# Optimization experiments

Hardware: AMD Instinct MI355X
Metric: run time of the kernel (lower is better)

The kernel has to match this reference:

```python
import jax, jax.numpy as jnp
import numpy as np

D_MODEL = 512
NUM_HEADS = 8
D_HEAD = D_MODEL // NUM_HEADS
SCALE = 1.0 / np.sqrt(D_HEAD)


def setup_inputs() -> dict:
    key = jax.random.key(0)
    ks = jax.random.split(key, 16)
    B, T, D = 8, 1024, D_MODEL
    std = 1.0 / np.sqrt(D)
    inp = {
        'x': jax.random.normal(ks[0], (B, T, D), jnp.float32),
        'pos_enc': jax.random.normal(ks[1], (1, 2 * T - 1, D), jnp.float32),
        'Wq': jax.random.normal(ks[2], (D, D), jnp.float32) * std,
        'bq': jnp.zeros((D,), jnp.float32),
        'Wk': jax.random.normal(ks[3], (D, D), jnp.float32) * std,
        'bk': jnp.zeros((D,), jnp.float32),
        'Wv': jax.random.normal(ks[4], (D, D), jnp.float32) * std,
        'bv': jnp.zeros((D,), jnp.float32),
        'Wpos': jax.random.normal(ks[5], (D, D), jnp.float32) * std,
        'pos_bias_u': jax.random.normal(ks[6], (NUM_HEADS, D_HEAD), jnp.float32) * std,
        'pos_bias_v': jax.random.normal(ks[7], (NUM_HEADS, D_HEAD), jnp.float32) * std,
        'Wo': jax.random.normal(ks[8], (D, D), jnp.float32) * std,
        'bo': jnp.zeros((D,), jnp.float32),
    }
    return inp


def _relative_shift(x):
    # x: (batch, heads, time, 2*time-1) -> (batch, heads, time, time)
    b, h, t, _ = x.shape
    x = jnp.pad(x, ((0, 0), (0, 0), (0, 0), (1, 0)))  # (b,h,t,2t)
    x = x.reshape(b, h, 2 * t, t)
    x = x[:, :, 1:, :]
    x = x.reshape(b, h, t, 2 * t - 1)
    return x[:, :, :, :t]


def reference(x, pos_enc, Wq, bq, Wk, bk, Wv, bv, Wpos, pos_bias_u, pos_bias_v, Wo, bo):
    B, T, D = x.shape
    H, Dh = NUM_HEADS, D_HEAD
    q = (x @ Wq + bq).reshape(B, T, H, Dh).transpose(0, 2, 1, 3)  # (B,H,T,Dh)
    k = (x @ Wk + bk).reshape(B, T, H, Dh).transpose(0, 2, 1, 3)
    v = (x @ Wv + bv).reshape(B, T, H, Dh).transpose(0, 2, 1, 3)
    p = (pos_enc @ Wpos).reshape(1, -1, H, Dh).transpose(0, 2, 1, 3)  # (1,H,2T-1,Dh)

    q_u = q + pos_bias_u[None, :, None, :]
    q_v = q + pos_bias_v[None, :, None, :]

    content_score = jnp.einsum('bhtd,bhsd->bhts', q_u, k)         # (B,H,T,T)
    pos_score = jnp.einsum('bhtd,xhpd->bhtp', q_v, p)             # (B,H,T,2T-1)
    pos_score = _relative_shift(pos_score)                         # (B,H,T,T)

    scores = (content_score + pos_score) * SCALE
    attn = jax.nn.softmax(scores, axis=-1)
    out = jnp.einsum('bhts,bhsd->bhtd', attn, v)                   # (B,H,T,Dh)
    out = out.transpose(0, 2, 1, 3).reshape(B, T, D)
    return out @ Wo + bo
```

## Files before the change

kernel.cpp:

```cpp
#include <hip/hip_runtime.h>
#include <hip/hip_bf16.h>

#define T_SEQ 1024
#define D_MODEL 512
#define N_HEADS 8
#define D_HEAD 64
#define KSCALE 0.1803368801111244f

typedef unsigned short ushort_t;
typedef short s16x8 __attribute__((ext_vector_type(8)));
typedef float f32x4 __attribute__((ext_vector_type(4)));

__device__ inline f32x4 mfma16(s16x8 a, s16x8 b, f32x4 c) {
    return __builtin_amdgcn_mfma_f32_16x16x32_bf16(a, b, c, 0, 0, 0);
}

__device__ inline ushort_t f2bf(float f) {
    union { float f; unsigned u; } v; v.f = f;
    unsigned r = v.u + 0x7FFFu + ((v.u >> 16) & 1u);
    return (ushort_t)(r >> 16);
}
__device__ inline float bf2f(short s) {
    union { unsigned u; float f; } t; t.u = ((unsigned)(unsigned short)s) << 16; return t.f;
}
__device__ inline void cvt4(const float4 f, ushort_t* t) {
    t[0] = f2bf(f.x); t[1] = f2bf(f.y); t[2] = f2bf(f.z); t[3] = f2bf(f.w);
}
__device__ inline s16x8 pack8(const ushort_t* t) {
    s16x8 r;
    #pragma unroll
    for (int e = 0; e < 8; ++e) r[e] = (short)t[e];
    return r;
}

__device__ inline int lidx(int row, int chunk) {
    return row * 64 + ((chunk ^ (row & 7)) << 3);
}

__device__ inline void gl_lds16(const ushort_t* g, ushort_t* l) {
    __builtin_amdgcn_global_load_lds(
        (const __attribute__((address_space(1))) unsigned*)g,
        (__attribute__((address_space(3))) unsigned*)l, 16, 0, 0);
}

__global__ __launch_bounds__(256) void prep(
    const float* __restrict__ x, const float* __restrict__ pos,
    const float* __restrict__ W0, const float* __restrict__ W1,
    const float* __restrict__ W2, const float* __restrict__ W3,
    const float* __restrict__ W4,
    ushort_t* __restrict__ xb, ushort_t* __restrict__ posb,
    ushort_t* __restrict__ WT)
{
    __shared__ float T[64][68];
    const int bx = blockIdx.x;
    const int tid = threadIdx.x;
    if (bx < 2560) {
        const size_t N1 = (size_t)8192 * 512;
        size_t e = ((size_t)bx * 256 + tid) * 8;
        ushort_t tmp[8];
        if (e < N1) {
            const float4* s = (const float4*)(x + e);
            cvt4(s[0], tmp); cvt4(s[1], tmp + 4);
            *(s16x8*)(xb + e) = pack8(tmp);
        } else {
            size_t e2 = e - N1;
            int row = (int)(e2 >> 9);
            if (row < 2047) {
                const float4* s = (const float4*)(pos + e2);
                cvt4(s[0], tmp); cvt4(s[1], tmp + 4);
            } else {
                #pragma unroll
                for (int i = 0; i < 8; ++i) tmp[i] = 0;
            }
            *(s16x8*)(posb + e2) = pack8(tmp);
        }
    } else {
        const int bz = bx - 2560;
        const int z = bz >> 6;
        const int rem = bz & 63;
        const int n0 = (rem & 7) * 64, k0 = (rem >> 3) * 64;
        const float* W = (z == 0) ? W0 : (z == 1) ? W1
                       : (z == 2) ? W2 : (z == 3) ? W3 : W4;
        const int rr = tid >> 2, cc = (tid & 3) * 16;

        const float* src = W + (size_t)(k0 + rr) * 512 + n0 + cc;
        *(float4*)&T[rr][cc + 0]  = *(const float4*)(src);
        *(float4*)&T[rr][cc + 4]  = *(const float4*)(src + 4);
        *(float4*)&T[rr][cc + 8]  = *(const float4*)(src + 8);
        *(float4*)&T[rr][cc + 12] = *(const float4*)(src + 12);
        __syncthreads();

        ushort_t tmp[16];
        #pragma unroll
        for (int e = 0; e < 16; ++e) tmp[e] = f2bf(T[cc + e][rr]);
        ushort_t* dst = WT + ((size_t)z * 512 + n0 + rr) * 512 + k0 + cc;
        *(s16x8*)dst       = pack8(tmp);
        *(s16x8*)(dst + 8) = pack8(tmp + 8);
    }
}

__global__ __launch_bounds__(256) void gemm_qkvp(
    const ushort_t* __restrict__ xb, const ushort_t* __restrict__ posb,
    const ushort_t* __restrict__ WT,
    const float* __restrict__ bq, const float* __restrict__ bk,
    const float* __restrict__ bv, const float* __restrict__ pbu,
    ushort_t* __restrict__ Qu, ushort_t* __restrict__ Ko,
    ushort_t* __restrict__ VoT, ushort_t* __restrict__ Po)
{
    const int tid = threadIdx.x;
    const bool is_p = (blockIdx.x == 12);
    int row0, col0;
    const ushort_t* A;
    const ushort_t* B;
    if (is_p) {
        row0 = ((int)blockIdx.y >> 2) * 128;
        col0 = ((int)blockIdx.y & 3) * 128;
        A = posb;
        B = WT + (size_t)3 * 512 * 512;
    } else {
        row0 = blockIdx.y * 128;
        col0 = blockIdx.x * 128;
        A = xb;
        B = WT;
    }
    const int w = tid >> 6, lane = tid & 63;
    const int quad = lane >> 4, lanelo = lane & 15;
    const int wr = w >> 1, wc = w & 1;

    __shared__ ushort_t AsF[128 * 64];
    __shared__ ushort_t BsF[128 * 64];

    f32x4 acc[4][4] = {};

    for (int k0 = 0; k0 < 512; k0 += 64) {
        __syncthreads();
        #pragma unroll
        for (int i = 0; i < 4; ++i) {
            const int L = i * 256 + tid;
            const int r = L >> 3, j = (L & 7) * 8;
            ushort_t* lbase = AsF + (size_t)(i * 256 + (tid & ~63)) * 8;
            gl_lds16(A + (size_t)(row0 + r) * 512 + k0 + j, lbase);
            ushort_t* lbase2 = BsF + (size_t)(i * 256 + (tid & ~63)) * 8;
            gl_lds16(B + (size_t)(col0 + r) * 512 + k0 + j, lbase2);
        }
        __syncthreads();

        #pragma unroll
        for (int ks = 0; ks < 2; ++ks) {
            s16x8 af[4], bf[4];
            #pragma unroll
            for (int i = 0; i < 4; ++i)
                af[i] = *(const s16x8*)(AsF + (size_t)(64 * wr + 16 * i + lanelo) * 64 + ks * 32 + quad * 8);
            #pragma unroll
            for (int j = 0; j < 4; ++j)
                bf[j] = *(const s16x8*)(BsF + (size_t)(64 * wc + 16 * j + lanelo) * 64 + ks * 32 + quad * 8);
            #pragma unroll
            for (int i = 0; i < 4; ++i)
                #pragma unroll
                for (int j = 0; j < 4; ++j)
                    acc[i][j] = mfma16(af[i], bf[j], acc[i][j]);
        }
    }

    if (is_p) {
        #pragma unroll
        for (int j = 0; j < 4; ++j) {
            int c = col0 + 64 * wc + 16 * j + lanelo;
            #pragma unroll
            for (int i = 0; i < 4; ++i)
                #pragma unroll
                for (int r = 0; r < 4; ++r) {
                    int row = row0 + 64 * wr + 16 * i + 4 * quad + r;
                    Po[(size_t)row * 512 + c] = f2bf(acc[i][j][r]);
                }
        }
        return;
    }

    const int set = col0 >> 9;
    const int cbase = (col0 & 511) + 64 * wc;
    if (set == 0) {
        #pragma unroll
        for (int j = 0; j < 4; ++j) {
            int c = cbase + 16 * j + lanelo;
            float vq = bq[c] + pbu[c];
            #pragma unroll
            for (int i = 0; i < 4; ++i)
                #pragma unroll
                for (int r = 0; r < 4; ++r) {
                    int row = row0 + 64 * wr + 16 * i + 4 * quad + r;
                    Qu[(size_t)row * 512 + c] = f2bf((acc[i][j][r] + vq) * KSCALE);
                }
        }
    } else if (set == 1) {
        #pragma unroll
        for (int j = 0; j < 4; ++j) {
            int c = cbase + 16 * j + lanelo;
            float vbk = bk[c];
            #pragma unroll
            for (int i = 0; i < 4; ++i)
                #pragma unroll
                for (int r = 0; r < 4; ++r) {
                    int row = row0 + 64 * wr + 16 * i + 4 * quad + r;
                    Ko[(size_t)row * 512 + c] = f2bf(acc[i][j][r] + vbk);
                }
        }
    } else {
        const int b_idx = row0 >> 10;
        #pragma unroll
        for (int j = 0; j < 4; ++j) {
            int c = cbase + 16 * j + lanelo;
            int hh = c >> 6, d = c & 63;
            float vbb = bv[c];
            #pragma unroll
            for (int i = 0; i < 4; ++i) {
                int t = (row0 & 1023) + 64 * wr + 16 * i + 4 * quad;
                ushort4 vp;
                vp.x = f2bf(acc[i][j][0] + vbb);
                vp.y = f2bf(acc[i][j][1] + vbb);
                vp.z = f2bf(acc[i][j][2] + vbb);
                vp.w = f2bf(acc[i][j][3] + vbb);
                *(ushort4*)(VoT + ((size_t)((b_idx * 8 + hh) * 64 + d)) * 1024 + t) = vp;
            }
        }
    }
}

__global__ __launch_bounds__(256) void attn_mfma(
    const ushort_t* __restrict__ Qu,
    const ushort_t* __restrict__ Kb, const ushort_t* __restrict__ VT,
    const ushort_t* __restrict__ Pb,
    const float* __restrict__ pbu, const float* __restrict__ pbv,
    ushort_t* __restrict__ AOb)
{
    const int tid = threadIdx.x;
    const int t0 = blockIdx.x * 64;
    const int h  = blockIdx.y;
    const int b  = blockIdx.z;
    const int w = tid >> 6, lane = tid & 63;
    const int quad = lane >> 4, lanelo = lane & 15;
    const int sr = tid >> 2;
    const int scch = (tid & 3) * 2;
    const int sc = scch * 8;

    __shared__ ushort_t Kt[64 * 64];
    __shared__ ushort_t VtT[64 * 64];
    __shared__ ushort_t Pt[128 * 64];
    __shared__ ushort_t Ps[64 * 64];

    const size_t qrow = (size_t)(b * T_SEQ + t0 + 16 * w + lanelo) * 512 + h * 64;
    s16x8 qu[2], qv[2];
    qu[0] = *(const s16x8*)(Qu + qrow + quad * 8);
    qu[1] = *(const s16x8*)(Qu + qrow + 32 + quad * 8);
    #pragma unroll
    for (int e = 0; e < 8; ++e) {
        int k0i = h * 64 + quad * 8 + e;
        float d0 = (pbv[k0i] - pbu[k0i]) * KSCALE;
        float d1 = (pbv[k0i + 32] - pbu[k0i + 32]) * KSCALE;
        qv[0][e] = (short)f2bf(bf2f(qu[0][e]) + d0);
        qv[1][e] = (short)f2bf(bf2f(qu[1][e]) + d1);
    }

    f32x4 acc_o[4] = {};
    float l_part[4] = {0.f, 0.f, 0.f, 0.f};

    const int u_base = lanelo + 63 - 4 * quad;
    const ushort_t* VTbh = VT + ((size_t)((b * 8 + h) * 64)) * 1024;
    const ushort_t* Kbh  = Kb + (size_t)b * T_SEQ * 512 + (size_t)h * 64;
    const int pr_base = 960 - t0;

    {
        const ushort_t* kp = Kbh + (size_t)sr * 512 + sc;
        *(s16x8*)(Kt + lidx(sr, scch))     = *(const s16x8*)kp;
        *(s16x8*)(Kt + lidx(sr, scch + 1)) = *(const s16x8*)(kp + 8);
        const ushort_t* vp = VTbh + (size_t)sr * 1024 + sc;
        *(s16x8*)(VtT + lidx(sr, scch))     = *(const s16x8*)vp;
        *(s16x8*)(VtT + lidx(sr, scch + 1)) = *(const s16x8*)(vp + 8);
        const int pr_r = tid >> 1, pc0 = (tid & 1) * 4;
        const int slot = (pr_base + pr_r) & 127;
        const ushort_t* gp = Pb + (size_t)(pr_base + pr_r) * 512 + h * 64 + pc0 * 8;
        *(s16x8*)(Pt + lidx(slot, pc0))     = *(const s16x8*)(gp +  0);
        *(s16x8*)(Pt + lidx(slot, pc0 + 1)) = *(const s16x8*)(gp +  8);
        *(s16x8*)(Pt + lidx(slot, pc0 + 2)) = *(const s16x8*)(gp + 16);
        *(s16x8*)(Pt + lidx(slot, pc0 + 3)) = *(const s16x8*)(gp + 24);
    }

    for (int it = 0; it < 16; ++it) {
        const int s0 = it * 64;
        __syncthreads();

        s16x8 kp0, kp1, vp0, vp1, pp0, pp1;
        const bool more = (it < 15);
        if (more) {
            const ushort_t* kp = Kbh + (size_t)(s0 + 64 + sr) * 512 + sc;
            kp0 = *(const s16x8*)kp;
            kp1 = *(const s16x8*)(kp + 8);
            const ushort_t* vp = VTbh + (size_t)sr * 1024 + s0 + 64 + sc;
            vp0 = *(const s16x8*)vp;
            vp1 = *(const s16x8*)(vp + 8);
            const ushort_t* gp = Pb + (size_t)(pr_base + s0 + 128 + sr) * 512 + h * 64 + sc;
            pp0 = *(const s16x8*)gp;
            pp1 = *(const s16x8*)(gp + 8);
        }

        const int pbase = (pr_base + s0) & 127;
        f32x4 acc_c[4] = {};
        f32x4 acc_g[5] = {};
        #pragma unroll
        for (int ks = 0; ks < 2; ++ks) {
            #pragma unroll
            for (int tn = 0; tn < 4; ++tn) {
                s16x8 kf = *(const s16x8*)(Kt + lidx(tn * 16 + lanelo, 4 * ks + quad));
                acc_c[tn] = mfma16(qu[ks], kf, acc_c[tn]);
            }
            #pragma unroll
            for (int i = 0; i < 5; ++i) {
                int prow = (pbase + (3 - w + i) * 16 + lanelo) & 127;
                s16x8 pf = *(const s16x8*)(Pt + lidx(prow, 4 * ks + quad));
                acc_g[i] = mfma16(qv[ks], pf, acc_g[i]);
            }
        }

        float p[4][4];
        #pragma unroll
        for (int r = 0; r < 4; ++r) {
            int u = u_base - r;
            int srcl = (quad << 4) | (u & 15);
            bool hi = (u >= 64);
            #pragma unroll
            for (int tn = 0; tn < 4; ++tn) {
                float v0 = __shfl(acc_g[tn][r], srcl);
                float v1 = __shfl(acc_g[tn + 1][r], srcl);
                float e = __builtin_amdgcn_exp2f(acc_c[tn][r] + (hi ? v1 : v0));
                p[tn][r] = e;
                l_part[r] += e;
            }
        }
        #pragma unroll
        for (int tn = 0; tn < 4; ++tn)
            #pragma unroll
            for (int r = 0; r < 4; ++r) {
                int pr = 16 * w + 4 * quad + r;
                int ch = 2 * tn + (lanelo >> 3);
                Ps[pr * 64 + ((ch ^ (pr & 7)) << 3) + (lanelo & 7)] = f2bf(p[tn][r]);
            }
        asm volatile("s_waitcnt lgkmcnt(0)" ::: "memory");

        #pragma unroll
        for (int ks = 0; ks < 2; ++ks) {
            s16x8 af = *(const s16x8*)(Ps + lidx(16 * w + lanelo, 4 * ks + quad));
            #pragma unroll
            for (int dt = 0; dt < 4; ++dt) {
                s16x8 vb = *(const s16x8*)(VtT + lidx(dt * 16 + lanelo, 4 * ks + quad));
                acc_o[dt] = mfma16(af, vb, acc_o[dt]);
            }
        }

        __syncthreads();
        if (more) {
            *(s16x8*)(Kt + lidx(sr, scch))      = kp0;
            *(s16x8*)(Kt + lidx(sr, scch + 1))  = kp1;
            *(s16x8*)(VtT + lidx(sr, scch))     = vp0;
            *(s16x8*)(VtT + lidx(sr, scch + 1)) = vp1;
            const int slot = (pr_base + s0 + 128 + sr) & 127;
            *(s16x8*)(Pt + lidx(slot, scch))     = pp0;
            *(s16x8*)(Pt + lidx(slot, scch + 1)) = pp1;
        }
    }

    float inv[4];
    #pragma unroll
    for (int r = 0; r < 4; ++r) {
        float l = l_part[r];
        l += __shfl_xor(l, 1);
        l += __shfl_xor(l, 2);
        l += __shfl_xor(l, 4);
        l += __shfl_xor(l, 8);
        inv[r] = 1.0f / l;
    }

    __syncthreads();
    #pragma unroll
    for (int r = 0; r < 4; ++r)
        #pragma unroll
        for (int dt = 0; dt < 4; ++dt) {
            int pr = 16 * w + 4 * quad + r;
            int ch = 2 * dt + (lanelo >> 3);
            Ps[pr * 64 + ((ch ^ (pr & 7)) << 3) + (lanelo & 7)] = f2bf(acc_o[dt][r] * inv[r]);
        }
    __syncthreads();
    {
        ushort_t* dst = AOb + (size_t)(b * T_SEQ + t0 + sr) * 512 + h * 64 + sc;
        *(s16x8*)dst       = *(const s16x8*)(Ps + lidx(sr, scch));
        *(s16x8*)(dst + 8) = *(const s16x8*)(Ps + lidx(sr, scch + 1));
    }
}

__global__ __launch_bounds__(256) void gemm_out(
    const ushort_t* __restrict__ A, const ushort_t* __restrict__ WTo,
    const float* __restrict__ bias, float* __restrict__ C)
{
    const int tid = threadIdx.x;
    const int col0 = blockIdx.x * 128;
    const int row0 = blockIdx.y * 128;
    const int w = tid >> 6, lane = tid & 63;
    const int quad = lane >> 4, lanelo = lane & 15;
    const int wr = w >> 1, wc = w & 1;

    __shared__ ushort_t AsF[128 * 64];
    __shared__ ushort_t BsF[128 * 64];

    f32x4 acc[4][4] = {};

    for (int k0 = 0; k0 < 512; k0 += 64) {
        __syncthreads();
        #pragma unroll
        for (int i = 0; i < 4; ++i) {
            const int L = i * 256 + tid;
            const int r = L >> 3, j = (L & 7) * 8;
            ushort_t* lbase = AsF + (size_t)(i * 256 + (tid & ~63)) * 8;
            gl_lds16(A + (size_t)(row0 + r) * 512 + k0 + j, lbase);
            ushort_t* lbase2 = BsF + (size_t)(i * 256 + (tid & ~63)) * 8;
            gl_lds16(WTo + (size_t)(col0 + r) * 512 + k0 + j, lbase2);
        }
        __syncthreads();

        #pragma unroll
        for (int ks = 0; ks < 2; ++ks) {
            s16x8 af[4], bf[4];
            #pragma unroll
            for (int i = 0; i < 4; ++i)
                af[i] = *(const s16x8*)(AsF + (size_t)(64 * wr + 16 * i + lanelo) * 64 + ks * 32 + quad * 8);
            #pragma unroll
            for (int j = 0; j < 4; ++j)
                bf[j] = *(const s16x8*)(BsF + (size_t)(64 * wc + 16 * j + lanelo) * 64 + ks * 32 + quad * 8);
            #pragma unroll
            for (int i = 0; i < 4; ++i)
                #pragma unroll
                for (int j = 0; j < 4; ++j)
                    acc[i][j] = mfma16(af[i], bf[j], acc[i][j]);
        }
    }

    #pragma unroll
    for (int j = 0; j < 4; ++j) {
        int c = col0 + 64 * wc + 16 * j + lanelo;
        float vb = bias[c];
        #pragma unroll
        for (int i = 0; i < 4; ++i)
            #pragma unroll
            for (int r = 0; r < 4; ++r) {
                int row = row0 + 64 * wr + 16 * i + 4 * quad + r;
                C[(size_t)row * 512 + c] = acc[i][j][r] + vb;
            }
    }
}

extern "C" void kernel_launch(void* const* d_in, const int* in_sizes, int n_in,
                              void* d_out, int out_size, void* d_ws, size_t ws_size,
                              hipStream_t stream) {
    const float* x       = (const float*)d_in[0];
    const float* pos_enc = (const float*)d_in[1];
    const float* Wq      = (const float*)d_in[2];
    const float* bq      = (const float*)d_in[3];
    const float* Wk      = (const float*)d_in[4];
    const float* bk      = (const float*)d_in[5];
    const float* Wv      = (const float*)d_in[6];
    const float* bv      = (const float*)d_in[7];
    const float* Wpos    = (const float*)d_in[8];
    const float* pbu     = (const float*)d_in[9];
    const float* pbv     = (const float*)d_in[10];
    const float* Wo      = (const float*)d_in[11];
    const float* bo      = (const float*)d_in[12];
    float* out = (float*)d_out;

    const size_t M  = 8 * T_SEQ;
    const size_t SZ = M * D_MODEL;

    char* ws = (char*)d_ws;
    ushort_t* xb   = (ushort_t*)ws;              ws += SZ * 2;
    ushort_t* posb = (ushort_t*)ws;              ws += (size_t)2048 * 512 * 2;
    ushort_t* Qu_b = (ushort_t*)ws;              ws += SZ * 2;
    ushort_t* K_b  = (ushort_t*)ws;              ws += SZ * 2;
    ushort_t* VT_b = (ushort_t*)ws;              ws += SZ * 2;
    ushort_t* P_b  = (ushort_t*)ws;              ws += (size_t)2048 * 512 * 2;
    ushort_t* WT   = (ushort_t*)ws;              ws += (size_t)5 * 512 * 512 * 2;
    ushort_t* AOb  = (ushort_t*)ws;              ws += SZ * 2;

    dim3 blk(256);

    hipLaunchKernelGGL(prep, dim3(2880), blk, 0, stream,
                       x, pos_enc, Wq, Wk, Wv, Wpos, Wo, xb, posb, WT);

    hipLaunchKernelGGL(gemm_qkvp, dim3(13, 64), blk, 0, stream,
                       xb, posb, WT, bq, bk, bv, pbu,
                       Qu_b, K_b, VT_b, P_b);

    hipLaunchKernelGGL(attn_mfma, dim3(16, 8, 8), blk, 0, stream,
                       Qu_b, K_b, VT_b, P_b, pbu, pbv, AOb);

    hipLaunchKernelGGL(gemm_out, dim3(4, 64), blk, 0, stream,
                       AOb, WT + (size_t)4 * 512 * 512, bo, out);
}
```

Before: 207.4 us.

## Enlarge attention query tile, double-buffer K/V/P via direct-to-LDS loads, remap blocks for XCD locality

The attention kernel now processes 128 query rows per block, two 16-row tiles per wave, so each K, V and positional fragment read from LDS feeds twice as many MFMAs. K/V are double-buffered and the positional window is a 256-row ring, both filled by asynchronous global-to-LDS loads instead of staging through registers, which removes one barrier per iteration. MFMA sections are bracketed with s_setprio, and launch bounds request 2 blocks per CU. All three GEMM/attention grids are flattened and remapped so consecutive blocks on the same XCD share data. The trade-off is more LDS and registers per block and half as many attention blocks.

```diff
diff --git a/kernel.cpp b/kernel.cpp
--- a/kernel.cpp
+++ b/kernel.cpp
@@ -108,18 +108,22 @@
     ushort_t* __restrict__ VoT, ushort_t* __restrict__ Po)
 {
     const int tid = threadIdx.x;
-    const bool is_p = (blockIdx.x == 12);
+    const int flat = blockIdx.x;
+    const int nf = (flat & 7) * 104 + (flat >> 3);
+    const int bxi = nf % 13, byi = nf / 13;
+
+    const bool is_p = (bxi == 12);
     int row0, col0;
     const ushort_t* A;
     const ushort_t* B;
     if (is_p) {
-        row0 = ((int)blockIdx.y >> 2) * 128;
-        col0 = ((int)blockIdx.y & 3) * 128;
+        row0 = (byi >> 2) * 128;
+        col0 = (byi & 3) * 128;
         A = posb;
         B = WT + (size_t)3 * 512 * 512;
     } else {
-        row0 = blockIdx.y * 128;
-        col0 = blockIdx.x * 128;
+        row0 = byi * 128;
+        col0 = bxi * 128;
         A = xb;
         B = WT;
     }
@@ -226,7 +230,7 @@
     }
 }
 
-__global__ __launch_bounds__(256) void attn_mfma(
+__global__ __launch_bounds__(256, 2) void attn_mfma(
     const ushort_t* __restrict__ Qu,
     const ushort_t* __restrict__ Kb, const ushort_t* __restrict__ VT,
     const ushort_t* __restrict__ Pb,
@@ -234,165 +238,192 @@
     ushort_t* __restrict__ AOb)
 {
     const int tid = threadIdx.x;
-    const int t0 = blockIdx.x * 64;
-    const int h  = blockIdx.y;
-    const int b  = blockIdx.z;
+    const int flat = blockIdx.x;
+    const int nf = (flat & 7) * 64 + (flat >> 3);
+    const int t0 = (nf & 7) * 128;
+    const int h  = (nf >> 3) & 7;
+    const int b  = nf >> 6;
+
     const int w = tid >> 6, lane = tid & 63;
     const int quad = lane >> 4, lanelo = lane & 15;
-    const int sr = tid >> 2;
-    const int scch = (tid & 3) * 2;
-    const int sc = scch * 8;
-
-    __shared__ ushort_t Kt[64 * 64];
-    __shared__ ushort_t VtT[64 * 64];
-    __shared__ ushort_t Pt[128 * 64];
-    __shared__ ushort_t Ps[64 * 64];
-
-    const size_t qrow = (size_t)(b * T_SEQ + t0 + 16 * w + lanelo) * 512 + h * 64;
-    s16x8 qu[2], qv[2];
-    qu[0] = *(const s16x8*)(Qu + qrow + quad * 8);
-    qu[1] = *(const s16x8*)(Qu + qrow + 32 + quad * 8);
+
+    __shared__ ushort_t Kt[2 * 64 * 64];
+    __shared__ ushort_t VtT[2 * 64 * 64];
+    __shared__ ushort_t Pt[256 * 64];
+    __shared__ ushort_t Ps[128 * 64];
+
+    const size_t qr0 = (size_t)(b * T_SEQ + t0 + 32 * w + lanelo) * 512 + h * 64;
+    s16x8 qu0[2], qu1[2], qv0[2], qv1[2];
+    qu0[0] = *(const s16x8*)(Qu + qr0 + quad * 8);
+    qu0[1] = *(const s16x8*)(Qu + qr0 + 32 + quad * 8);
+    qu1[0] = *(const s16x8*)(Qu + qr0 + (size_t)16 * 512 + quad * 8);
+    qu1[1] = *(const s16x8*)(Qu + qr0 + (size_t)16 * 512 + 32 + quad * 8);
     #pragma unroll
     for (int e = 0; e < 8; ++e) {
         int k0i = h * 64 + quad * 8 + e;
         float d0 = (pbv[k0i] - pbu[k0i]) * KSCALE;
         float d1 = (pbv[k0i + 32] - pbu[k0i + 32]) * KSCALE;
-        qv[0][e] = (short)f2bf(bf2f(qu[0][e]) + d0);
-        qv[1][e] = (short)f2bf(bf2f(qu[1][e]) + d1);
-    }
-
-    f32x4 acc_o[4] = {};
-    float l_part[4] = {0.f, 0.f, 0.f, 0.f};
-
-    const int u_base = lanelo + 63 - 4 * quad;
+        qv0[0][e] = (short)f2bf(bf2f(qu0[0][e]) + d0);
+        qv0[1][e] = (short)f2bf(bf2f(qu0[1][e]) + d1);
+        qv1[0][e] = (short)f2bf(bf2f(qu1[0][e]) + d0);
+        qv1[1][e] = (short)f2bf(bf2f(qu1[1][e]) + d1);
+    }
+
+    f32x4 acc_o[2][4] = {};
+    float l_part[2][4] = {{0.f,0.f,0.f,0.f},{0.f,0.f,0.f,0.f}};
+
     const ushort_t* VTbh = VT + ((size_t)((b * 8 + h) * 64)) * 1024;
     const ushort_t* Kbh  = Kb + (size_t)b * T_SEQ * 512 + (size_t)h * 64;
     const int pr_base = 960 - t0;
 
     {
-        const ushort_t* kp = Kbh + (size_t)sr * 512 + sc;
-        *(s16x8*)(Kt + lidx(sr, scch))     = *(const s16x8*)kp;
-        *(s16x8*)(Kt + lidx(sr, scch + 1)) = *(const s16x8*)(kp + 8);
-        const ushort_t* vp = VTbh + (size_t)sr * 1024 + sc;
-        *(s16x8*)(VtT + lidx(sr, scch))     = *(const s16x8*)vp;
-        *(s16x8*)(VtT + lidx(sr, scch + 1)) = *(const s16x8*)(vp + 8);
-        const int pr_r = tid >> 1, pc0 = (tid & 1) * 4;
-        const int slot = (pr_base + pr_r) & 127;
-        const ushort_t* gp = Pb + (size_t)(pr_base + pr_r) * 512 + h * 64 + pc0 * 8;
-        *(s16x8*)(Pt + lidx(slot, pc0))     = *(const s16x8*)(gp +  0);
-        *(s16x8*)(Pt + lidx(slot, pc0 + 1)) = *(const s16x8*)(gp +  8);
-        *(s16x8*)(Pt + lidx(slot, pc0 + 2)) = *(const s16x8*)(gp + 16);
-        *(s16x8*)(Pt + lidx(slot, pc0 + 3)) = *(const s16x8*)(gp + 24);
-    }
+        #pragma unroll
+        for (int i = 0; i < 2; ++i) {
+            const int L = i * 256 + tid;
+            const int r = L >> 3;
+            const int ch = (L & 7) ^ (r & 7);
+            gl_lds16(Kbh + (size_t)r * 512 + ch * 8,
+                     Kt + (size_t)(i * 256 + (tid & ~63)) * 8);
+            gl_lds16(VTbh + (size_t)r * 1024 + ch * 8,
+                     VtT + (size_t)(i * 256 + (tid & ~63)) * 8);
+        }
+        const int g0p = pr_base - 64;
+        #pragma unroll
+        for (int i = 0; i < 6; ++i) {
+            const int L = i * 256 + tid;
+            const int gr = g0p + (L >> 3);
+            const int ch = (L & 7) ^ (gr & 7);
+            const int sgb = (g0p + ((i * 256 + (tid & ~63)) >> 3)) & 255;
+            gl_lds16(Pb + (size_t)gr * 512 + h * 64 + ch * 8,
+                     Pt + (size_t)sgb * 64);
+        }
+    }
+    __syncthreads();
 
     for (int it = 0; it < 16; ++it) {
         const int s0 = it * 64;
+        const int cur = it & 1;
+
+        if (it < 15) {
+            ushort_t* Kn = Kt + (cur ^ 1) * 4096;
+            ushort_t* Vn = VtT + (cur ^ 1) * 4096;
+            const int sn = s0 + 64;
+            #pragma unroll
+            for (int i = 0; i < 2; ++i) {
+                const int L = i * 256 + tid;
+                const int r = L >> 3;
+                const int ch = (L & 7) ^ (r & 7);
+                gl_lds16(Kbh + (size_t)(sn + r) * 512 + ch * 8,
+                         Kn + (size_t)(i * 256 + (tid & ~63)) * 8);
+                gl_lds16(VTbh + (size_t)r * 1024 + sn + ch * 8,
+                         Vn + (size_t)(i * 256 + (tid & ~63)) * 8);
+            }
+            const int g0 = pr_base + s0 + 128;
+            #pragma unroll
+            for (int i = 0; i < 2; ++i) {
+                const int L = i * 256 + tid;
+                const int gr = g0 + (L >> 3);
+                const int ch = (L & 7) ^ (gr & 7);
+                const int sgb = (g0 + ((i * 256 + (tid & ~63)) >> 3)) & 255;
+                gl_lds16(Pb + (size_t)gr * 512 + h * 64 + ch * 8,
+                         Pt + (size_t)sgb * 64);
+            }
+        }
+
+        const ushort_t* Kc = Kt + cur * 4096;
+        const ushort_t* Vc = VtT + cur * 4096;
+        const int pb = (pr_base + s0) & 255;
+
+        f32x4 acc_c[2][4] = {};
+        f32x4 acc_g[2][5] = {};
+        __builtin_amdgcn_s_setprio(1);
+        #pragma unroll
+        for (int ks = 0; ks < 2; ++ks) {
+            #pragma unroll
+            for (int tn = 0; tn < 4; ++tn) {
+                s16x8 kf = *(const s16x8*)(Kc + lidx(tn * 16 + lanelo, 4 * ks + quad));
+                acc_c[0][tn] = mfma16(qu0[ks], kf, acc_c[0][tn]);
+                acc_c[1][tn] = mfma16(qu1[ks], kf, acc_c[1][tn]);
+            }
+            #pragma unroll
+            for (int m = 0; m < 6; ++m) {
+                int prow = (pb + 256 + (2 - 2 * w + m) * 16 + lanelo) & 255;
+                s16x8 pf = *(const s16x8*)(Pt + lidx(prow, 4 * ks + quad));
+                if (m >= 1) acc_g[0][m - 1] = mfma16(qv0[ks], pf, acc_g[0][m - 1]);
+                if (m <= 4) acc_g[1][m]     = mfma16(qv1[ks], pf, acc_g[1][m]);
+            }
+        }
+        __builtin_amdgcn_s_setprio(0);
+
+        #pragma unroll
+        for (int rt = 0; rt < 2; ++rt) {
+            #pragma unroll
+            for (int r = 0; r < 4; ++r) {
+                const int u = lanelo + 15 - 4 * quad - r;
+                const int srcl = (quad << 4) | (u & 15);
+                const bool hi = (u >= 16);
+                #pragma unroll
+                for (int tn = 0; tn < 4; ++tn) {
+                    float v0 = __shfl(acc_g[rt][tn][r], srcl);
+                    float v1 = __shfl(acc_g[rt][tn + 1][r], srcl);
+                    float e = __builtin_amdgcn_exp2f(acc_c[rt][tn][r] + (hi ? v1 : v0));
+                    l_part[rt][r] += e;
+                    const int pr = 32 * w + 16 * rt + 4 * quad + r;
+                    const int ch = 2 * tn + (lanelo >> 3);
+                    Ps[pr * 64 + ((ch ^ (pr & 7)) << 3) + (lanelo & 7)] = f2bf(e);
+                }
+            }
+        }
+        asm volatile("s_waitcnt lgkmcnt(0)" ::: "memory");
+
+        __builtin_amdgcn_s_setprio(1);
+        #pragma unroll
+        for (int ks = 0; ks < 2; ++ks) {
+            s16x8 af0 = *(const s16x8*)(Ps + lidx(32 * w + lanelo, 4 * ks + quad));
+            s16x8 af1 = *(const s16x8*)(Ps + lidx(32 * w + 16 + lanelo, 4 * ks + quad));
+            #pragma unroll
+            for (int dt = 0; dt < 4; ++dt) {
+                s16x8 vb = *(const s16x8*)(Vc + lidx(dt * 16 + lanelo, 4 * ks + quad));
+                acc_o[0][dt] = mfma16(af0, vb, acc_o[0][dt]);
+                acc_o[1][dt] = mfma16(af1, vb, acc_o[1][dt]);
+            }
+        }
+        __builtin_amdgcn_s_setprio(0);
+
         __syncthreads();
-
-        s16x8 kp0, kp1, vp0, vp1, pp0, pp1;
-        const bool more = (it < 15);
-        if (more) {
-            const ushort_t* kp = Kbh + (size_t)(s0 + 64 + sr) * 512 + sc;
-            kp0 = *(const s16x8*)kp;
-            kp1 = *(const s16x8*)(kp + 8);
-            const ushort_t* vp = VTbh + (size_t)sr * 1024 + s0 + 64 + sc;
-            vp0 = *(const s16x8*)vp;
-            vp1 = *(const s16x8*)(vp + 8);
-            const ushort_t* gp = Pb + (size_t)(pr_base + s0 + 128 + sr) * 512 + h * 64 + sc;
-            pp0 = *(const s16x8*)gp;
-            pp1 = *(const s16x8*)(gp + 8);
-        }
-
-        const int pbase = (pr_base + s0) & 127;
-        f32x4 acc_c[4] = {};
-        f32x4 acc_g[5] = {};
-        #pragma unroll
-        for (int ks = 0; ks < 2; ++ks) {
-            #pragma unroll
-            for (int tn = 0; tn < 4; ++tn) {
-                s16x8 kf = *(const s16x8*)(Kt + lidx(tn * 16 + lanelo, 4 * ks + quad));
-                acc_c[tn] = mfma16(qu[ks], kf, acc_c[tn]);
-            }
-            #pragma unroll
-            for (int i = 0; i < 5; ++i) {
-                int prow = (pbase + (3 - w + i) * 16 + lanelo) & 127;
-                s16x8 pf = *(const s16x8*)(Pt + lidx(prow, 4 * ks + quad));
-                acc_g[i] = mfma16(qv[ks], pf, acc_g[i]);
-            }
-        }
-
-        float p[4][4];
+    }
+
+    float inv[2][4];
+    #pragma unroll
+    for (int rt = 0; rt < 2; ++rt)
         #pragma unroll
         for (int r = 0; r < 4; ++r) {
-            int u = u_base - r;
-            int srcl = (quad << 4) | (u & 15);
-            bool hi = (u >= 64);
-            #pragma unroll
-            for (int tn = 0; tn < 4; ++tn) {
-                float v0 = __shfl(acc_g[tn][r], srcl);
-                float v1 = __shfl(acc_g[tn + 1][r], srcl);
-                float e = __builtin_amdgcn_exp2f(acc_c[tn][r] + (hi ? v1 : v0));
-                p[tn][r] = e;
-                l_part[r] += e;
-            }
-        }
-        #pragma unroll
-        for (int tn = 0; tn < 4; ++tn)
+            float l = l_part[rt][r];
+            l += __shfl_xor(l, 1);
+            l += __shfl_xor(l, 2);
+            l += __shfl_xor(l, 4);
+            l += __shfl_xor(l, 8);
+            inv[rt][r] = 1.0f / l;
+        }
+
+    #pragma unroll
+    for (int rt = 0; rt < 2; ++rt)
+        #pragma unroll
+        for (int dt = 0; dt < 4; ++dt)
             #pragma unroll
             for (int r = 0; r < 4; ++r) {
-                int pr = 16 * w + 4 * quad + r;
-                int ch = 2 * tn + (lanelo >> 3);
-                Ps[pr * 64 + ((ch ^ (pr & 7)) << 3) + (lanelo & 7)] = f2bf(p[tn][r]);
-            }
-        asm volatile("s_waitcnt lgkmcnt(0)" ::: "memory");
-
-        #pragma unroll
-        for (int ks = 0; ks < 2; ++ks) {
-            s16x8 af = *(const s16x8*)(Ps + lidx(16 * w + lanelo, 4 * ks + quad));
-            #pragma unroll
-            for (int dt = 0; dt < 4; ++dt) {
-                s16x8 vb = *(const s16x8*)(VtT + lidx(dt * 16 + lanelo, 4 * ks + quad));
-                acc_o[dt] = mfma16(af, vb, acc_o[dt]);
-            }
-        }
-
-        __syncthreads();
-        if (more) {
-            *(s16x8*)(Kt + lidx(sr, scch))      = kp0;
-            *(s16x8*)(Kt + lidx(sr, scch + 1))  = kp1;
-            *(s16x8*)(VtT + lidx(sr, scch))     = vp0;
-            *(s16x8*)(VtT + lidx(sr, scch + 1)) = vp1;
-            const int slot = (pr_base + s0 + 128 + sr) & 127;
-            *(s16x8*)(Pt + lidx(slot, scch))     = pp0;
-            *(s16x8*)(Pt + lidx(slot, scch + 1)) = pp1;
-        }
-    }
-
-    float inv[4];
-    #pragma unroll
-    for (int r = 0; r < 4; ++r) {
-        float l = l_part[r];
-        l += __shfl_xor(l, 1);
-        l += __shfl_xor(l, 2);
-        l += __shfl_xor(l, 4);
-        l += __shfl_xor(l, 8);
-        inv[r] = 1.0f / l;
-    }
-
-    __syncthreads();
-    #pragma unroll
-    for (int r = 0; r < 4; ++r)
-        #pragma unroll
-        for (int dt = 0; dt < 4; ++dt) {
-            int pr = 16 * w + 4 * quad + r;
-            int ch = 2 * dt + (lanelo >> 3);
-            Ps[pr * 64 + ((ch ^ (pr & 7)) << 3) + (lanelo & 7)] = f2bf(acc_o[dt][r] * inv[r]);
-        }
+                const int pr = 32 * w + 16 * rt + 4 * quad + r;
+                const int ch = 2 * dt + (lanelo >> 3);
+                Ps[pr * 64 + ((ch ^ (pr & 7)) << 3) + (lanelo & 7)] =
+                    f2bf(acc_o[rt][dt][r] * inv[rt][r]);
+            }
     __syncthreads();
     {
-        ushort_t* dst = AOb + (size_t)(b * T_SEQ + t0 + sr) * 512 + h * 64 + sc;
-        *(s16x8*)dst       = *(const s16x8*)(Ps + lidx(sr, scch));
-        *(s16x8*)(dst + 8) = *(const s16x8*)(Ps + lidx(sr, scch + 1));
+        const int row = tid >> 1, cb = (tid & 1) * 4;
+        ushort_t* dst = AOb + (size_t)(b * T_SEQ + t0 + row) * 512 + h * 64 + cb * 8;
+        #pragma unroll
+        for (int c = 0; c < 4; ++c)
+            *(s16x8*)(dst + c * 8) = *(const s16x8*)(Ps + lidx(row, cb + c));
     }
 }
 
@@ -401,8 +432,10 @@
     const float* __restrict__ bias, float* __restrict__ C)
 {
     const int tid = threadIdx.x;
-    const int col0 = blockIdx.x * 128;
-    const int row0 = blockIdx.y * 128;
+    const int flat = blockIdx.x;
+    const int nfi = (flat & 7) * 32 + (flat >> 3);
+    const int col0 = (nfi & 3) * 128;
+    const int row0 = (nfi >> 2) * 128;
     const int w = tid >> 6, lane = tid & 63;
     const int quad = lane >> 4, lanelo = lane & 15;
     const int wr = w >> 1, wc = w & 1;
@@ -492,13 +525,13 @@
     hipLaunchKernelGGL(prep, dim3(2880), blk, 0, stream,
                        x, pos_enc, Wq, Wk, Wv, Wpos, Wo, xb, posb, WT);
 
-    hipLaunchKernelGGL(gemm_qkvp, dim3(13, 64), blk, 0, stream,
+    hipLaunchKernelGGL(gemm_qkvp, dim3(832), blk, 0, stream,
                        xb, posb, WT, bq, bk, bv, pbu,
                        Qu_b, K_b, VT_b, P_b);
 
-    hipLaunchKernelGGL(attn_mfma, dim3(16, 8, 8), blk, 0, stream,
+    hipLaunchKernelGGL(attn_mfma, dim3(512), blk, 0, stream,
                        Qu_b, K_b, VT_b, P_b, pbu, pbv, AOb);
 
-    hipLaunchKernelGGL(gemm_out, dim3(4, 64), blk, 0, stream,
+    hipLaunchKernelGGL(gemm_out, dim3(256), blk, 0, stream,
                        AOb, WT + (size_t)4 * 512 * 512, bo, out);
 }
```

New measurement: 191.6 us. 1.08x faster.
